# Kernel optimization log

Measured on AMD Instinct MI355X. Metric: run time of the kernel, lower is better.

## Reference

```python
import jax, jax.numpy as jnp
import numpy as np

B, T, C = 2, 2048, 2048
H, HD = 16, 128  # num_heads, head_dim; inner_dim = H*HD = C
EPS = 1e-8


def _hadamard(n):
    # Sylvester construction, orthonormal scaling 1/sqrt(n)
    h = np.array([[1.0]], dtype=np.float32)
    while h.shape[0] < n:
        h = np.block([[h, h], [h, -h]])
    return jnp.asarray(h / np.sqrt(n), dtype=jnp.float32)


def _round_ste(x):
    # straight-through rounding (matches int8 training-time quantization semantics)
    return x + jax.lax.stop_gradient(jnp.round(x) - x)


def q8_linear(x, w):
    # dynamic per-token int8 activation quant + per-out-channel int8 weight quant
    s_x = jnp.max(jnp.abs(x), axis=-1, keepdims=True) / 127.0 + EPS   # (B,T,1)
    xq = _round_ste(jnp.clip(x / s_x, -127.0, 127.0))
    s_w = jnp.max(jnp.abs(w), axis=-1, keepdims=True) / 127.0 + EPS   # (O,1)
    wq = _round_ste(jnp.clip(w / s_w, -127.0, 127.0))
    return jnp.einsum('btk,ok->bto', xq, wq) * s_x * s_w[:, 0]


def rmsnorm(x, g, eps=1e-6):
    return x * jax.lax.rsqrt(jnp.mean(x * x, axis=-1, keepdims=True) + eps) * g


def apply_rope(x, cos, sin):
    # x: (B,T,H*HD); cos/sin: (T,HD/2); interleaved rotary per head
    b, t, c = x.shape
    xh = x.reshape(b, t, -1, HD)
    x1, x2 = xh[..., 0::2], xh[..., 1::2]
    co = cos[None, :, None, :]
    si = sin[None, :, None, :]
    o1 = x1 * co - x2 * si
    o2 = x1 * si + x2 * co
    out = jnp.stack([o1, o2], axis=-1).reshape(b, t, -1, HD)
    return out.reshape(b, t, c)


def setup_inputs() -> dict:
    key = jax.random.key(0)
    ks = jax.random.split(key, 8)
    hidden_states = jax.random.normal(ks[0], (B, T, C), jnp.float32)
    attention_mask = jax.random.randint(ks[1], (B,), 1, T + 1).astype(jnp.int32)  # valid lengths
    sc = 1.0 / np.sqrt(C)
    wq = jax.random.normal(ks[2], (H * HD, C), jnp.float32) * sc
    wk = jax.random.normal(ks[3], (H * HD, C), jnp.float32) * sc
    wv = jax.random.normal(ks[4], (H * HD, C), jnp.float32) * sc
    wo = jax.random.normal(ks[5], (C, H * HD), jnp.float32) * (1.0 / np.sqrt(H * HD))
    q_gamma = jnp.ones((H * HD,), jnp.float32)
    k_gamma = jnp.ones((H * HD,), jnp.float32)
    inv_freq = 1.0 / (10000.0 ** (np.arange(0, HD, 2, dtype=np.float32) / HD))
    freqs = np.outer(np.arange(T, dtype=np.float32), inv_freq)  # (T, HD/2)
    cos = jnp.asarray(np.cos(freqs), jnp.float32)
    sin = jnp.asarray(np.sin(freqs), jnp.float32)
    return {"hidden_states": hidden_states, "attention_mask": attention_mask,
            "wq": wq, "wk": wk, "wv": wv, "wo": wo,
            "q_gamma": q_gamma, "k_gamma": k_gamma, "cos": cos, "sin": sin}


def reference(hidden_states, attention_mask, wq, wk, wv, wo, q_gamma, k_gamma, cos, sin):
    b, t, c = hidden_states.shape
    q = rmsnorm(q8_linear(hidden_states, wq), q_gamma)
    k = rmsnorm(q8_linear(hidden_states, wk), k_gamma)
    v = q8_linear(hidden_states, wv)
    q = apply_rope(q, cos, sin)
    k = apply_rope(k, cos, sin)
    # (B,T,H*HD) -> (B,H,T,HD)
    q = q.reshape(b, t, H, HD).transpose(0, 2, 1, 3)
    k = k.reshape(b, t, H, HD).transpose(0, 2, 1, 3)
    v = v.reshape(b, t, H, HD).transpose(0, 2, 1, 3)
    # Hadamard rotation of q/k head dims (orthonormal -> preserves qk dot products)
    Hm = _hadamard(HD)
    qh = q @ Hm
    kh = k @ Hm
    scores = jnp.einsum('bhqd,bhkd->bhqk', qh, kh) * (1.0 / np.sqrt(HD))
    # ragged batch mask: keys beyond per-batch valid length are masked out
    valid = jnp.arange(t)[None, :] < attention_mask[:, None]   # (B,T)
    scores = jnp.where(valid[:, None, None, :], scores, -1e9)
    p = jax.nn.softmax(scores, axis=-1)
    o = jnp.einsum('bhqk,bhkd->bhqd', p, v)
    o = o.transpose(0, 2, 1, 3).reshape(b, t, c)
    return q8_linear(o, wo)
```

## Files before the change

kernel.cpp:

```cpp
#include <hip/hip_runtime.h>
#include <stdint.h>

typedef unsigned short u16;
typedef unsigned int u32;
typedef int v4i __attribute__((ext_vector_type(4)));
typedef float v4f __attribute__((ext_vector_type(4)));
typedef short v8s __attribute__((ext_vector_type(8)));

#define Bn 2
#define Tn 2048
#define Cn 2048
#define Hn 16
#define HDn 128

__device__ __forceinline__ float b2f(u16 u) {
    u32 x = ((u32)u) << 16;
    float f;
    __builtin_memcpy(&f, &x, 4);
    return f;
}
__device__ __forceinline__ u16 f2b(float f) {
    u32 x;
    __builtin_memcpy(&x, &f, 4);
    u32 r = (x + 0x7fffu + ((x >> 16) & 1u)) >> 16;
    return (u16)r;
}

__device__ __forceinline__ void async16(const void* g, void* l) {
    __builtin_amdgcn_global_load_lds(
        (const __attribute__((address_space(1))) u32*)g,
        (__attribute__((address_space(3))) u32*)l, 16, 0, 0);
}

__global__ __launch_bounds__(256) void quant_all(
    const float* __restrict__ w0, const float* __restrict__ w1,
    const float* __restrict__ w2, const float* __restrict__ w3,
    const float* __restrict__ hid, int8_t* __restrict__ Q,
    float* __restrict__ S) {
    int r = blockIdx.x;
    const float* src;
    int ro;
    if (r < 2048) { src = w0; ro = r; }
    else if (r < 4096) { src = w1; ro = r - 2048; }
    else if (r < 6144) { src = w2; ro = r - 4096; }
    else if (r < 8192) { src = w3; ro = r - 6144; }
    else { src = hid; ro = r - 8192; }
    const float* x = src + (size_t)ro * Cn;
    int tid = threadIdx.x;
    float4 v0 = ((const float4*)x)[tid * 2];
    float4 v1 = ((const float4*)x)[tid * 2 + 1];
    float a[8] = {v0.x, v0.y, v0.z, v0.w, v1.x, v1.y, v1.z, v1.w};
    float m = 0.f;
#pragma unroll
    for (int i = 0; i < 8; i++) m = fmaxf(m, fabsf(a[i]));
#pragma unroll
    for (int o = 32; o; o >>= 1) m = fmaxf(m, __shfl_xor(m, o));
    __shared__ float sm[4];
    if ((tid & 63) == 0) sm[tid >> 6] = m;
    __syncthreads();
    m = fmaxf(fmaxf(sm[0], sm[1]), fmaxf(sm[2], sm[3]));
    float s = m * (1.0f / 127.0f) + 1e-8f;
    if (tid == 0) S[r] = s;
    u32 lo = 0, hi = 0;
#pragma unroll
    for (int i = 0; i < 8; i++) {
        float q = rintf(fminf(127.f, fmaxf(-127.f, a[i] / s)));
        int qi = (int)q;
        u32 byte = (u32)(qi & 0xff);
        if (i < 4) lo |= byte << (8 * i);
        else hi |= byte << (8 * (i - 4));
    }
    u32* qp = (u32*)(Q + (size_t)r * Cn);
    qp[tid * 2] = lo;
    qp[tid * 2 + 1] = hi;
}

__global__ __launch_bounds__(256) void quant_rows(const float* __restrict__ X,
                                                  int8_t* __restrict__ Q,
                                                  float* __restrict__ S) {
    int r = blockIdx.x;
    const float* x = X + (size_t)r * Cn;
    int tid = threadIdx.x;
    float4 v0 = ((const float4*)x)[tid * 2];
    float4 v1 = ((const float4*)x)[tid * 2 + 1];
    float a[8] = {v0.x, v0.y, v0.z, v0.w, v1.x, v1.y, v1.z, v1.w};
    float m = 0.f;
#pragma unroll
    for (int i = 0; i < 8; i++) m = fmaxf(m, fabsf(a[i]));
#pragma unroll
    for (int o = 32; o; o >>= 1) m = fmaxf(m, __shfl_xor(m, o));
    __shared__ float sm[4];
    if ((tid & 63) == 0) sm[tid >> 6] = m;
    __syncthreads();
    m = fmaxf(fmaxf(sm[0], sm[1]), fmaxf(sm[2], sm[3]));
    float s = m * (1.0f / 127.0f) + 1e-8f;
    if (tid == 0) S[r] = s;
    u32 lo = 0, hi = 0;
#pragma unroll
    for (int i = 0; i < 8; i++) {
        float q = rintf(fminf(127.f, fmaxf(-127.f, a[i] / s)));
        int qi = (int)q;
        u32 byte = (u32)(qi & 0xff);
        if (i < 4) lo |= byte << (8 * i);
        else hi |= byte << (8 * (i - 4));
    }
    u32* qp = (u32*)(Q + (size_t)r * Cn);
    qp[tid * 2] = lo;
    qp[tid * 2 + 1] = hi;
}

__global__ __launch_bounds__(256) void gemm_i8(
    const int8_t* __restrict__ A, const int8_t* __restrict__ Bw,
    const float* __restrict__ sA, const float* __restrict__ sB,
    void* __restrict__ Co, long long bStride, long long sbStride,
    long long cStride, int fp32out) {
    int z = blockIdx.z;
    Bw += (size_t)z * bStride;
    sB += (size_t)z * sbStride;
    const int K = 2048, N = 2048;
    __shared__ int8_t As[128 * 64];
    __shared__ int8_t Bs[128 * 64];
    int m0 = blockIdx.x * 128, n0 = blockIdx.y * 128;
    int tid = threadIdx.x, w = tid >> 6, lane = tid & 63;
    int quad = lane >> 4, l15 = lane & 15;
    int wy = w >> 1, wx = w & 1;
    const v4i zi = {0, 0, 0, 0};
    v4i acc[4][4];
#pragma unroll
    for (int i = 0; i < 4; i++)
#pragma unroll
        for (int j = 0; j < 4; j++) acc[i][j] = zi;
    int lrow = lane >> 2;
    int slot = lane & 3;
    int srow = w * 32 + lrow;
    int klog = ((slot ^ (lrow & 3)) * 16);
    const int8_t* ga = A + (size_t)(m0 + srow) * K + klog;
    const int8_t* gb = Bw + (size_t)(n0 + srow) * K + klog;
    int8_t* la = &As[srow * 64 + slot * 16];
    int8_t* lb = &Bs[srow * 64 + slot * 16];
    for (int k0 = 0; k0 < K; k0 += 64) {
        async16(ga + k0, la);
        async16(ga + k0 + (size_t)16 * K, la + 16 * 64);
        async16(gb + k0, lb);
        async16(gb + k0 + (size_t)16 * K, lb + 16 * 64);
        __syncthreads();
        int swz = (quad ^ (l15 & 3)) * 16;
        v4i af[4], bf4[4];
#pragma unroll
        for (int i = 0; i < 4; i++)
            af[i] = *(const v4i*)&As[(wy * 64 + i * 16 + l15) * 64 + swz];
#pragma unroll
        for (int j = 0; j < 4; j++)
            bf4[j] = *(const v4i*)&Bs[(wx * 64 + j * 16 + l15) * 64 + swz];
#pragma unroll
        for (int i = 0; i < 4; i++)
#pragma unroll
            for (int j = 0; j < 4; j++)
                acc[i][j] = __builtin_amdgcn_mfma_i32_16x16x64_i8(
                    af[i], bf4[j], acc[i][j], 0, 0, 0);
        __syncthreads();
    }
#pragma unroll
    for (int i = 0; i < 4; i++) {
        int mb = m0 + wy * 64 + i * 16 + quad * 4;
        float s0 = sA[mb], s1 = sA[mb + 1], s2 = sA[mb + 2], s3 = sA[mb + 3];
#pragma unroll
        for (int j = 0; j < 4; j++) {
            int n = n0 + wx * 64 + j * 16 + l15;
            float sb = sB[n];
            if (fp32out) {
                float* cp = (float*)Co + (size_t)cStride * z + (size_t)mb * N + n;
                cp[0] = (float)acc[i][j][0] * s0 * sb;
                cp[N] = (float)acc[i][j][1] * s1 * sb;
                cp[2 * N] = (float)acc[i][j][2] * s2 * sb;
                cp[3 * N] = (float)acc[i][j][3] * s3 * sb;
            } else {
                u16* cp = (u16*)Co + (size_t)cStride * z + (size_t)mb * N + n;
                cp[0] = f2b((float)acc[i][j][0] * s0 * sb);
                cp[N] = f2b((float)acc[i][j][1] * s1 * sb);
                cp[2 * N] = f2b((float)acc[i][j][2] * s2 * sb);
                cp[3 * N] = f2b((float)acc[i][j][3] * s3 * sb);
            }
        }
    }
}

__global__ __launch_bounds__(256) void norm_rope2(u16* __restrict__ Qb,
                                                  u16* __restrict__ Kb,
                                                  const float* __restrict__ qg,
                                                  const float* __restrict__ kg,
                                                  const float* __restrict__ cs,
                                                  const float* __restrict__ sn) {
    int row = blockIdx.x;
    int isq = row < 4096;
    row &= 4095;
    u16* x = (isq ? Qb : Kb) + (size_t)row * Cn;
    const float* g = isq ? qg : kg;
    float ps = isq ? 0.08838834764831845f : 1.0f;
    int t = row & (Tn - 1);
    int tid = threadIdx.x;
    uint4 raw = ((const uint4*)x)[tid];
    u16 us[8];
    us[0] = raw.x & 0xffff; us[1] = raw.x >> 16;
    us[2] = raw.y & 0xffff; us[3] = raw.y >> 16;
    us[4] = raw.z & 0xffff; us[5] = raw.z >> 16;
    us[6] = raw.w & 0xffff; us[7] = raw.w >> 16;
    float v[8];
#pragma unroll
    for (int i = 0; i < 8; i++) v[i] = b2f(us[i]);
    float ss = 0.f;
#pragma unroll
    for (int i = 0; i < 8; i++) ss += v[i] * v[i];
#pragma unroll
    for (int o = 32; o; o >>= 1) ss += __shfl_xor(ss, o);
    __shared__ float sm[4];
    if ((tid & 63) == 0) sm[tid >> 6] = ss;
    __syncthreads();
    ss = sm[0] + sm[1] + sm[2] + sm[3];
    float r = rsqrtf(ss * (1.f / 2048.f) + 1e-6f) * ps;
    float4 g0 = ((const float4*)g)[tid * 2];
    float4 g1 = ((const float4*)g)[tid * 2 + 1];
    float n[8];
    n[0] = v[0] * r * g0.x; n[1] = v[1] * r * g0.y;
    n[2] = v[2] * r * g0.z; n[3] = v[3] * r * g0.w;
    n[4] = v[4] * r * g1.x; n[5] = v[5] * r * g1.y;
    n[6] = v[6] * r * g1.z; n[7] = v[7] * r * g1.w;
    int pi = (tid & 15) * 4;
    float4 c4 = *(const float4*)(cs + t * 64 + pi);
    float4 s4 = *(const float4*)(sn + t * 64 + pi);
    float o[8];
    o[0] = n[0] * c4.x - n[1] * s4.x; o[1] = n[0] * s4.x + n[1] * c4.x;
    o[2] = n[2] * c4.y - n[3] * s4.y; o[3] = n[2] * s4.y + n[3] * c4.y;
    o[4] = n[4] * c4.z - n[5] * s4.z; o[5] = n[4] * s4.z + n[5] * c4.z;
    o[6] = n[6] * c4.w - n[7] * s4.w; o[7] = n[6] * s4.w + n[7] * c4.w;
    uint4 out;
    out.x = (u32)f2b(o[0]) | ((u32)f2b(o[1]) << 16);
    out.y = (u32)f2b(o[2]) | ((u32)f2b(o[3]) << 16);
    out.z = (u32)f2b(o[4]) | ((u32)f2b(o[5]) << 16);
    out.w = (u32)f2b(o[6]) | ((u32)f2b(o[7]) << 16);
    ((uint4*)x)[tid] = out;
}

__global__ __launch_bounds__(256) void vtrans(const u16* __restrict__ V,
                                              u16* __restrict__ Vt) {
    int bh = blockIdx.y;
    int b = bh >> 4, h = bh & 15;
    int t0 = blockIdx.x * 64;
    __shared__ u32 tile[64][133];
    int tid = threadIdx.x;
    int r = tid >> 2, seg = (tid & 3) * 32;
    const uint4* src =
        (const uint4*)(V + ((size_t)b * Tn + t0 + r) * Cn + h * HDn + seg);
#pragma unroll
    for (int i = 0; i < 4; i++) {
        uint4 u = src[i];
        u32 uu[4] = {u.x, u.y, u.z, u.w};
#pragma unroll
        for (int j = 0; j < 4; j++) {
            tile[r][seg + i * 8 + j * 2] = uu[j] & 0xffff;
            tile[r][seg + i * 8 + j * 2 + 1] = uu[j] >> 16;
        }
    }
    __syncthreads();
    int d = tid >> 1, tseg = (tid & 1) * 32;
    u16* dst = Vt + ((size_t)bh * HDn + d) * Tn + t0 + tseg;
#pragma unroll
    for (int i = 0; i < 4; i++) {
        u32 p0 = tile[tseg + i * 8 + 0][d] | (tile[tseg + i * 8 + 1][d] << 16);
        u32 p1 = tile[tseg + i * 8 + 2][d] | (tile[tseg + i * 8 + 3][d] << 16);
        u32 p2 = tile[tseg + i * 8 + 4][d] | (tile[tseg + i * 8 + 5][d] << 16);
        u32 p3 = tile[tseg + i * 8 + 6][d] | (tile[tseg + i * 8 + 7][d] << 16);
        ((uint4*)dst)[i] = make_uint4(p0, p1, p2, p3);
    }
}

__global__ __launch_bounds__(256, 3) void flash(const u16* __restrict__ Qb,
                                                const u16* __restrict__ Kb,
                                                const u16* __restrict__ Vt,
                                                const int* __restrict__ mask,
                                                float* __restrict__ O) {
    int id = blockIdx.x;
    int bh = (id & 7) + 8 * (id >> 8);
    int qt = (id >> 3) & 31;
    int b = bh >> 4, h = bh & 15;
    int L = mask[b];
    int nkfull = L >> 6;
    int nk = (L + 63) >> 6;
    __shared__ u16 Ks[2][64 * 128];
    __shared__ u16 Ps[2][64 * 72];
    __shared__ float sred[256];
    __shared__ float sinv[64];
    int tid = threadIdx.x, w = tid >> 6, lane = tid & 63;
    int quad = lane >> 4, l15 = lane & 15;

    v8s aq[4][4];
#pragma unroll
    for (int i = 0; i < 4; i++)
#pragma unroll
        for (int kk = 0; kk < 4; kk++)
            aq[i][kk] = *(const v8s*)(Qb +
                                      ((size_t)b * Tn + qt * 64 + i * 16 + l15) * Cn +
                                      h * HDn + kk * 32 + quad * 8);

    const u16* ksp[4];
    int kdo[4];
#pragma unroll
    for (int cc = 0; cc < 4; cc++) {
        int c = w * 4 + cc;
        int rk = c * 4 + (lane >> 4);
        int sk = lane & 15;
        int lgk = sk ^ (rk & 7);
        ksp[cc] = Kb + ((size_t)b * Tn + rk) * Cn + h * HDn + lgk * 8;
        kdo[cc] = rk * 128 + sk * 8;
    }

    const u16* vp0 = Vt + ((size_t)bh * HDn + 2 * w * 16 + l15) * Tn + quad * 8;
    const u16* vp1 = vp0 + 16 * Tn;

    float sum16[16];
#pragma unroll
    for (int j = 0; j < 16; j++) sum16[j] = 0.f;
    const v4f zf = {0.f, 0.f, 0.f, 0.f};
    v4f oacc[4][2];
#pragma unroll
    for (int m = 0; m < 4; m++) {
        oacc[m][0] = zf;
        oacc[m][1] = zf;
    }

#pragma unroll
    for (int cc = 0; cc < 4; cc++) {
        async16(ksp[cc], &Ks[0][kdo[cc]]);
        ksp[cc] += (size_t)64 * Cn;
    }
    __syncthreads();

    int cur = 0;
    for (int kt = 0; kt < nk; kt++) {
        if (kt + 1 < nk) {
#pragma unroll
            for (int cc = 0; cc < 4; cc++) {
                async16(ksp[cc], &Ks[cur ^ 1][kdo[cc]]);
                ksp[cc] += (size_t)64 * Cn;
            }
        }
        v8s bv00 = *(const v8s*)(vp0);
        v8s bv10 = *(const v8s*)(vp0 + 32);
        v8s bv01 = *(const v8s*)(vp1);
        v8s bv11 = *(const v8s*)(vp1 + 32);
        vp0 += 64;
        vp1 += 64;
        v4f sacc[4] = {zf, zf, zf, zf};
        const u16* krow = &Ks[cur][(w * 16 + l15) * 128];
        __builtin_amdgcn_s_setprio(1);
#pragma unroll
        for (int kk = 0; kk < 4; kk++) {
            v8s bk = *(const v8s*)(krow + ((((kk * 4 + quad) ^ (l15 & 7))) << 3));
#pragma unroll
            for (int i = 0; i < 4; i++)
                sacc[i] = __builtin_amdgcn_mfma_f32_16x16x32_bf16(aq[i][kk], bk,
                                                                  sacc[i], 0, 0, 0);
        }
        __builtin_amdgcn_s_setprio(0);
        bool valid = (kt < nkfull) || ((kt * 64 + w * 16 + l15) < L);
#pragma unroll
        for (int i = 0; i < 4; i++)
#pragma unroll
            for (int r2 = 0; r2 < 4; r2++) {
                float p = valid ? __expf(sacc[i][r2]) : 0.f;
                sum16[i * 4 + r2] += p;
                Ps[cur][(i * 16 + quad * 4 + r2) * 72 + w * 16 + l15] = f2b(p);
            }
        __syncthreads();
        __builtin_amdgcn_s_setprio(1);
#pragma unroll
        for (int kk2 = 0; kk2 < 2; kk2++) {
            v8s ap[4];
#pragma unroll
            for (int m = 0; m < 4; m++)
                ap[m] = *(const v8s*)(&Ps[cur][(m * 16 + l15) * 72 + kk2 * 32 +
                                               quad * 8]);
            v8s bva = kk2 ? bv10 : bv00;
            v8s bvb = kk2 ? bv11 : bv01;
#pragma unroll
            for (int m = 0; m < 4; m++) {
                oacc[m][0] = __builtin_amdgcn_mfma_f32_16x16x32_bf16(
                    ap[m], bva, oacc[m][0], 0, 0, 0);
                oacc[m][1] = __builtin_amdgcn_mfma_f32_16x16x32_bf16(
                    ap[m], bvb, oacc[m][1], 0, 0, 0);
            }
        }
        __builtin_amdgcn_s_setprio(0);
        cur ^= 1;
    }
#pragma unroll
    for (int j = 0; j < 16; j++) {
        float s = sum16[j];
        s += __shfl_xor(s, 1);
        s += __shfl_xor(s, 2);
        s += __shfl_xor(s, 4);
        s += __shfl_xor(s, 8);
        sum16[j] = s;
    }
    if (l15 == 0) {
#pragma unroll
        for (int i = 0; i < 4; i++)
#pragma unroll
            for (int r2 = 0; r2 < 4; r2++)
                sred[w * 64 + i * 16 + quad * 4 + r2] = sum16[i * 4 + r2];
    }
    __syncthreads();
    if (tid < 64)
        sinv[tid] =
            1.f / (sred[tid] + sred[64 + tid] + sred[128 + tid] + sred[192 + tid]);
    __syncthreads();
#pragma unroll
    for (int m = 0; m < 4; m++)
#pragma unroll
        for (int r2 = 0; r2 < 4; r2++) {
            float inv = sinv[m * 16 + quad * 4 + r2];
            int row = qt * 64 + m * 16 + quad * 4 + r2;
#pragma unroll
            for (int nbi = 0; nbi < 2; nbi++) {
                int d = h * HDn + (2 * w + nbi) * 16 + l15;
                O[((size_t)b * Tn + row) * Cn + d] = oacc[m][nbi][r2] * inv;
            }
        }
}

extern "C" void kernel_launch(void* const* d_in, const int* in_sizes, int n_in,
                              void* d_out, int out_size, void* d_ws,
                              size_t ws_size, hipStream_t stream) {
    const float* hidden = (const float*)d_in[0];
    const int* mask = (const int*)d_in[1];
    const float* wq = (const float*)d_in[2];
    const float* wk = (const float*)d_in[3];
    const float* wv = (const float*)d_in[4];
    const float* wo = (const float*)d_in[5];
    const float* qg = (const float*)d_in[6];
    const float* kg = (const float*)d_in[7];
    const float* cs = (const float*)d_in[8];
    const float* sn = (const float*)d_in[9];

    char* ws = (char*)d_ws;
    int8_t* q8 = (int8_t*)(ws);
    float* sAll = (float*)(ws + 25165824);
    u16* qb = (u16*)(ws + 25214976);
    u16* kb = (u16*)(ws + 41992192);
    u16* vb = (u16*)(ws + 58769408);
    u16* vt = (u16*)(ws + 75546624);
    float* Obuf = (float*)(ws + 92323840);
    int8_t* hid8 = q8 + 16777216;
    float* sx = sAll + 8192;

    quant_all<<<12288, 256, 0, stream>>>(wq, wk, wv, wo, hidden, q8, sAll);

    gemm_i8<<<dim3(32, 16, 3), 256, 0, stream>>>(hid8, q8, sx, sAll, (void*)qb,
                                                 4194304LL, 2048LL, 8388608LL, 0);

    norm_rope2<<<8192, 256, 0, stream>>>(qb, kb, qg, kg, cs, sn);
    vtrans<<<dim3(32, 32), 256, 0, stream>>>(vb, vt);

    flash<<<dim3(1024), 256, 0, stream>>>(qb, kb, vt, mask, Obuf);

    quant_rows<<<4096, 256, 0, stream>>>(Obuf, hid8, sx);
    gemm_i8<<<dim3(32, 16, 1), 256, 0, stream>>>(hid8, q8 + 12582912, sx,
                                                 sAll + 6144, d_out, 0LL, 0LL,
                                                 0LL, 1);
}
```

Before: 345.7 us.

## Restructure flash attention so each wave owns 16 query rows end to end

The flash kernel is reorganized so each wave handles 16 query rows across all 64 keys and all 128 head dims, computing S transposed (K as A operand). P now stays in a per-wave LDS slice, so the block-wide P exchange and the cross-wave row-sum reduction go away. The Q scale now folds in log2(e), so exp2f replaces __expf, and bf16 packing uses v_cvt_pk_bf16_f32. In exchange each wave loads the full V tile (16 v8s registers per iteration), which raises register pressure and global V traffic per block.

```diff
diff --git a/kernel.cpp b/kernel.cpp
--- a/kernel.cpp
+++ b/kernel.cpp
@@ -24,6 +24,11 @@
     __builtin_memcpy(&x, &f, 4);
     u32 r = (x + 0x7fffu + ((x >> 16) & 1u)) >> 16;
     return (u16)r;
+}
+__device__ __forceinline__ u32 cvtpk(float a, float b) {
+    u32 r;
+    asm("v_cvt_pk_bf16_f32 %0, %1, %2" : "=v"(r) : "v"(a), "v"(b));
+    return r;
 }
 
 __device__ __forceinline__ void async16(const void* g, void* l) {
@@ -196,7 +201,7 @@
     row &= 4095;
     u16* x = (isq ? Qb : Kb) + (size_t)row * Cn;
     const float* g = isq ? qg : kg;
-    float ps = isq ? 0.08838834764831845f : 1.0f;
+    float ps = isq ? 0.1275174306f : 1.0f;
     int t = row & (Tn - 1);
     int tid = threadIdx.x;
     uint4 raw = ((const uint4*)x)[tid];
@@ -286,21 +291,18 @@
     int L = mask[b];
     int nkfull = L >> 6;
     int nk = (L + 63) >> 6;
+    int rem = L & 63;
     __shared__ u16 Ks[2][64 * 128];
-    __shared__ u16 Ps[2][64 * 72];
-    __shared__ float sred[256];
-    __shared__ float sinv[64];
+    __shared__ u16 Pw[4][16 * 64];
     int tid = threadIdx.x, w = tid >> 6, lane = tid & 63;
     int quad = lane >> 4, l15 = lane & 15;
-
-    v8s aq[4][4];
-#pragma unroll
-    for (int i = 0; i < 4; i++)
-#pragma unroll
-        for (int kk = 0; kk < 4; kk++)
-            aq[i][kk] = *(const v8s*)(Qb +
-                                      ((size_t)b * Tn + qt * 64 + i * 16 + l15) * Cn +
-                                      h * HDn + kk * 32 + quad * 8);
+    int sw = l15 & 7;
+
+    const u16* qrow =
+        Qb + ((size_t)b * Tn + qt * 64 + w * 16 + l15) * Cn + h * HDn + quad * 8;
+    v8s qf[4];
+#pragma unroll
+    for (int kk = 0; kk < 4; kk++) qf[kk] = *(const v8s*)(qrow + kk * 32);
 
     const u16* ksp[4];
     int kdo[4];
@@ -314,19 +316,13 @@
         kdo[cc] = rk * 128 + sk * 8;
     }
 
-    const u16* vp0 = Vt + ((size_t)bh * HDn + 2 * w * 16 + l15) * Tn + quad * 8;
-    const u16* vp1 = vp0 + 16 * Tn;
-
-    float sum16[16];
-#pragma unroll
-    for (int j = 0; j < 16; j++) sum16[j] = 0.f;
+    const u16* vrun = Vt + ((size_t)bh * HDn + l15) * Tn + quad * 8;
+
+    float rs = 0.f;
     const v4f zf = {0.f, 0.f, 0.f, 0.f};
-    v4f oacc[4][2];
-#pragma unroll
-    for (int m = 0; m < 4; m++) {
-        oacc[m][0] = zf;
-        oacc[m][1] = zf;
-    }
+    v4f oacc[8];
+#pragma unroll
+    for (int nb = 0; nb < 8; nb++) oacc[nb] = zf;
 
 #pragma unroll
     for (int cc = 0; cc < 4; cc++) {
@@ -337,6 +333,15 @@
 
     int cur = 0;
     for (int kt = 0; kt < nk; kt++) {
+        v8s vv[2][8];
+#pragma unroll
+        for (int ks = 0; ks < 2; ks++)
+#pragma unroll
+            for (int nb = 0; nb < 8; nb++)
+                vv[ks][nb] =
+                    *(const v8s*)(vrun + (size_t)(nb * 16) * Tn + ks * 32);
+        vrun += 64;
+        __builtin_amdgcn_sched_barrier(0);
         if (kt + 1 < nk) {
 #pragma unroll
             for (int cc = 0; cc < 4; cc++) {
@@ -344,88 +349,63 @@
                 ksp[cc] += (size_t)64 * Cn;
             }
         }
-        v8s bv00 = *(const v8s*)(vp0);
-        v8s bv10 = *(const v8s*)(vp0 + 32);
-        v8s bv01 = *(const v8s*)(vp1);
-        v8s bv11 = *(const v8s*)(vp1 + 32);
-        vp0 += 64;
-        vp1 += 64;
         v4f sacc[4] = {zf, zf, zf, zf};
-        const u16* krow = &Ks[cur][(w * 16 + l15) * 128];
-        __builtin_amdgcn_s_setprio(1);
+        const u16* kbase = &Ks[cur][0];
 #pragma unroll
         for (int kk = 0; kk < 4; kk++) {
-            v8s bk = *(const v8s*)(krow + ((((kk * 4 + quad) ^ (l15 & 7))) << 3));
-#pragma unroll
-            for (int i = 0; i < 4; i++)
-                sacc[i] = __builtin_amdgcn_mfma_f32_16x16x32_bf16(aq[i][kk], bk,
-                                                                  sacc[i], 0, 0, 0);
-        }
-        __builtin_amdgcn_s_setprio(0);
-        bool valid = (kt < nkfull) || ((kt * 64 + w * 16 + l15) < L);
-#pragma unroll
-        for (int i = 0; i < 4; i++)
-#pragma unroll
-            for (int r2 = 0; r2 < 4; r2++) {
-                float p = valid ? __expf(sacc[i][r2]) : 0.f;
-                sum16[i * 4 + r2] += p;
-                Ps[cur][(i * 16 + quad * 4 + r2) * 72 + w * 16 + l15] = f2b(p);
+#pragma unroll
+            for (int kb = 0; kb < 4; kb++) {
+                v8s kf = *(const v8s*)(kbase + (kb * 16 + l15) * 128 +
+                                       (((kk * 4 + quad) ^ sw) << 3));
+                sacc[kb] = __builtin_amdgcn_mfma_f32_16x16x32_bf16(
+                    kf, qf[kk], sacc[kb], 0, 0, 0);
             }
+        }
+#pragma unroll
+        for (int kb = 0; kb < 4; kb++) {
+            float p0, p1, p2, p3;
+            if (kt < nkfull) {
+                p0 = exp2f(sacc[kb][0]);
+                p1 = exp2f(sacc[kb][1]);
+                p2 = exp2f(sacc[kb][2]);
+                p3 = exp2f(sacc[kb][3]);
+            } else {
+                int key = kb * 16 + quad * 4;
+                p0 = (key + 0 < rem) ? exp2f(sacc[kb][0]) : 0.f;
+                p1 = (key + 1 < rem) ? exp2f(sacc[kb][1]) : 0.f;
+                p2 = (key + 2 < rem) ? exp2f(sacc[kb][2]) : 0.f;
+                p3 = (key + 3 < rem) ? exp2f(sacc[kb][3]) : 0.f;
+            }
+            rs += (p0 + p1) + (p2 + p3);
+            int ch = kb * 2 + (quad >> 1);
+            u32* dst = (u32*)&Pw[w][l15 * 64 + ((ch ^ sw) << 3) + ((quad & 1) << 2)];
+            dst[0] = cvtpk(p0, p1);
+            dst[1] = cvtpk(p2, p3);
+        }
+#pragma unroll
+        for (int ks = 0; ks < 2; ks++) {
+            v8s pa = *(const v8s*)&Pw[w][l15 * 64 + (((ks * 4 + quad) ^ sw) << 3)];
+#pragma unroll
+            for (int nb = 0; nb < 8; nb++)
+                oacc[nb] = __builtin_amdgcn_mfma_f32_16x16x32_bf16(
+                    pa, vv[ks][nb], oacc[nb], 0, 0, 0);
+        }
         __syncthreads();
-        __builtin_amdgcn_s_setprio(1);
-#pragma unroll
-        for (int kk2 = 0; kk2 < 2; kk2++) {
-            v8s ap[4];
-#pragma unroll
-            for (int m = 0; m < 4; m++)
-                ap[m] = *(const v8s*)(&Ps[cur][(m * 16 + l15) * 72 + kk2 * 32 +
-                                               quad * 8]);
-            v8s bva = kk2 ? bv10 : bv00;
-            v8s bvb = kk2 ? bv11 : bv01;
-#pragma unroll
-            for (int m = 0; m < 4; m++) {
-                oacc[m][0] = __builtin_amdgcn_mfma_f32_16x16x32_bf16(
-                    ap[m], bva, oacc[m][0], 0, 0, 0);
-                oacc[m][1] = __builtin_amdgcn_mfma_f32_16x16x32_bf16(
-                    ap[m], bvb, oacc[m][1], 0, 0, 0);
-            }
-        }
-        __builtin_amdgcn_s_setprio(0);
         cur ^= 1;
     }
-#pragma unroll
-    for (int j = 0; j < 16; j++) {
-        float s = sum16[j];
-        s += __shfl_xor(s, 1);
-        s += __shfl_xor(s, 2);
-        s += __shfl_xor(s, 4);
-        s += __shfl_xor(s, 8);
-        sum16[j] = s;
-    }
-    if (l15 == 0) {
-#pragma unroll
-        for (int i = 0; i < 4; i++)
-#pragma unroll
-            for (int r2 = 0; r2 < 4; r2++)
-                sred[w * 64 + i * 16 + quad * 4 + r2] = sum16[i * 4 + r2];
-    }
-    __syncthreads();
-    if (tid < 64)
-        sinv[tid] =
-            1.f / (sred[tid] + sred[64 + tid] + sred[128 + tid] + sred[192 + tid]);
-    __syncthreads();
-#pragma unroll
-    for (int m = 0; m < 4; m++)
-#pragma unroll
-        for (int r2 = 0; r2 < 4; r2++) {
-            float inv = sinv[m * 16 + quad * 4 + r2];
-            int row = qt * 64 + m * 16 + quad * 4 + r2;
-#pragma unroll
-            for (int nbi = 0; nbi < 2; nbi++) {
-                int d = h * HDn + (2 * w + nbi) * 16 + l15;
-                O[((size_t)b * Tn + row) * Cn + d] = oacc[m][nbi][r2] * inv;
-            }
-        }
+    rs += __shfl_xor(rs, 16);
+    rs += __shfl_xor(rs, 32);
+    float rinv = 1.f / rs;
+    float inv[4];
+#pragma unroll
+    for (int r2 = 0; r2 < 4; r2++) inv[r2] = __shfl(rinv, quad * 4 + r2, 16);
+    int qrow0 = qt * 64 + w * 16 + quad * 4;
+#pragma unroll
+    for (int r2 = 0; r2 < 4; r2++) {
+        float* orow = O + ((size_t)b * Tn + qrow0 + r2) * Cn + h * HDn + l15;
+#pragma unroll
+        for (int nb = 0; nb < 8; nb++) orow[nb * 16] = oacc[nb][r2] * inv[r2];
+    }
 }
 
 extern "C" void kernel_launch(void* const* d_in, const int* in_sizes, int n_in,
```

Measured after the change: 425.4 us. 1.23x slower.
